# Optimization experiments

Measured on AMD Instinct MI355X. Metric: run time of the kernel, lower is better.

Reference implementation:

```python
import jax, jax.numpy as jnp
import numpy as np

B, CTX_DIM, CTX_SIZE, HID, SEQLEN = 32, 1024, 2048, 1024, 64


def setup_inputs() -> dict:
    key = jax.random.key(0)
    k1, k2, k3, k4 = jax.random.split(key, 4)
    hidden = jax.random.normal(k1, (1, B, HID), dtype=jnp.float32)
    contextvects = jax.random.normal(k2, (B, CTX_DIM, CTX_SIZE), dtype=jnp.float32)
    # nn.Linear(context_dim, hidden_size): W is [hidden_size, context_dim]
    W = jax.random.normal(k3, (HID, CTX_DIM), dtype=jnp.float32) / np.sqrt(CTX_DIM)
    b = jax.random.normal(k4, (HID,), dtype=jnp.float32) * 0.01
    return {"seqlen": SEQLEN, "hidden": hidden, "contextvects": contextvects, "W": W, "b": b}


def reference(seqlen, hidden, contextvects, W, b):
    # Original torch loop recomputes the identical quantities every timestep;
    # compute once and broadcast across seqlen (same math, no redundancy).
    # contextvects: [B, D, C]; project each context position: [B, C, H]
    context_proj = jnp.einsum('bdc,hd->bch', contextvects, W) + b
    # hidden: [1, B, H] -> scores [B, C]
    scores = jnp.einsum('bch,bh->bc', context_proj, hidden[0])
    attn_weights = jax.nn.softmax(scores, axis=1)  # softmax over context positions
    ctx = jnp.einsum('bdc,bc->bd', contextvects, attn_weights)  # [B, D]
    return jnp.broadcast_to(ctx[None, :, :], (seqlen, ctx.shape[0], ctx.shape[1]))
```

## Files before the change

### kernel.cpp

```cpp
#include <hip/hip_runtime.h>
#include <math.h>

#define NB 32
#define ND 1024
#define NC 2048
#define NH 1024
#define NSEQ 64
#define CCHUNK 32
#define NCHUNK (NC / CCHUNK)

__global__ __launch_bounds__(128) void k1_v(const float* __restrict__ hidden,
                                            const float* __restrict__ W,
                                            float* __restrict__ v) {
  const int b = blockIdx.x >> 3;
  const int d = ((blockIdx.x & 7) << 7) + threadIdx.x;
  const float* hb = hidden + b * NH;
  float acc = 0.f;
#pragma unroll 16
  for (int h = 0; h < NH; ++h) acc += hb[h] * W[h * ND + d];
  v[b * ND + d] = acc;
}

__global__ __launch_bounds__(256) void k2_main(const float* __restrict__ ctx,
                                               const float* __restrict__ v,
                                               float* __restrict__ accp,
                                               float* __restrict__ ml) {
  __shared__ __align__(16) float tile[ND * CCHUNK];
  __shared__ __align__(16) float vs[ND];
  __shared__ __align__(16) float4 sred[256];
  __shared__ __align__(16) float pf[CCHUNK];

  const int t = threadIdx.x;
  const int bid = blockIdx.x;
  const int b = bid >> 6;
  const int c0 = (bid & 63) * CCHUNK;

  {
    float4 vv = *(const float4*)(v + b * ND + t * 4);
    *(float4*)(vs + t * 4) = vv;
  }
  __syncthreads();

  const int cg = t & 7;
  const int dp = t >> 3;
  const float* gp = ctx + (size_t)b * ND * NC + (size_t)dp * NC + c0 + cg * 4;
  float* tw = tile + dp * CCHUNK + cg * 4;
  float4 s4 = make_float4(0.f, 0.f, 0.f, 0.f);
#pragma unroll 8
  for (int j = 0; j < 32; ++j) {
    float4 x = *(const float4*)(gp + (size_t)32 * NC * j);
    *(float4*)(tw + 32 * CCHUNK * j) = x;
    float vd = vs[dp + 32 * j];
    s4.x += x.x * vd; s4.y += x.y * vd; s4.z += x.z * vd; s4.w += x.w * vd;
  }
  sred[t] = s4;
  __syncthreads();

  if (t < 32) {
    const float* sr = (const float*)sred;
    float s = 0.f;
#pragma unroll
    for (int p = 0; p < 32; ++p) s += sr[p * 32 + t];
    float mm = s;
#pragma unroll
    for (int off = 16; off; off >>= 1) mm = fmaxf(mm, __shfl_xor(mm, off, 32));
    float e = __expf(s - mm);
    float ls = e;
#pragma unroll
    for (int off = 16; off; off >>= 1) ls += __shfl_xor(ls, off, 32);
    pf[t] = e;
    if (t == 0) { ml[bid * 2] = mm; ml[bid * 2 + 1] = ls; }
  }
  __syncthreads();

  float4 pr[8];
#pragma unroll
  for (int j = 0; j < 8; ++j)
    pr[j] = *(const float4*)(pf + ((j + t) & 7) * 4);

  float* ao = accp + (size_t)bid * ND;
#pragma unroll
  for (int k = 0; k < 4; ++k) {
    const int d = t + 256 * k;
    const float* tr = tile + d * CCHUNK;
    float a = 0.f;
#pragma unroll
    for (int j = 0; j < 8; ++j) {
      const int jr = (j + t) & 7;
      float4 x = *(const float4*)(tr + jr * 4);
      float4 pp = pr[j];
      a += x.x * pp.x + x.y * pp.y + x.z * pp.z + x.w * pp.w;
    }
    ao[d] = a;
  }
}

__global__ __launch_bounds__(256) void k3_combine(const float* __restrict__ accp,
                                                  const float* __restrict__ ml,
                                                  float* __restrict__ ctxo) {
  __shared__ float sc[64];
  __shared__ float sinv;
  const int b = blockIdx.x >> 2;
  const int dq = blockIdx.x & 3;
  const int t = threadIdx.x;
  if (t < 64) {
    float mi = ml[(b * 64 + t) * 2];
    float li = ml[(b * 64 + t) * 2 + 1];
    float mg = mi;
#pragma unroll
    for (int off = 32; off; off >>= 1) mg = fmaxf(mg, __shfl_xor(mg, off, 64));
    float scale = __expf(mi - mg);
    float dpart = scale * li;
#pragma unroll
    for (int off = 32; off; off >>= 1) dpart += __shfl_xor(dpart, off, 64);
    sc[t] = scale;
    if (t == 0) sinv = 1.0f / dpart;
  }
  __syncthreads();
  const int d = dq * 256 + t;
  const float* ap = accp + (size_t)b * 64 * ND + d;
  float acc = 0.f;
#pragma unroll 8
  for (int i = 0; i < 64; ++i) acc += sc[i] * ap[i * ND];
  ctxo[b * ND + d] = acc * sinv;
}

__global__ __launch_bounds__(256) void k4_bcast(const float* __restrict__ ctxo,
                                               float* __restrict__ out) {
  const int sb = blockIdx.x;
  const int b = sb & 31;
  const int t = threadIdx.x;
  float4 x = *(const float4*)(ctxo + b * ND + t * 4);
  *(float4*)(out + (size_t)sb * ND + t * 4) = x;
}

extern "C" void kernel_launch(void* const* d_in, const int* in_sizes, int n_in,
                              void* d_out, int out_size, void* d_ws, size_t ws_size,
                              hipStream_t stream) {
  (void)in_sizes; (void)n_in; (void)out_size; (void)ws_size;
  const float* hidden = (const float*)d_in[1];
  const float* ctxv   = (const float*)d_in[2];
  const float* W      = (const float*)d_in[3];
  float* out = (float*)d_out;

  char* ws = (char*)d_ws;
  float* v    = (float*)(ws);
  float* ml   = (float*)(ws + 131072);
  float* ctxo = (float*)(ws + 147456);

  k1_v<<<256, 128, 0, stream>>>(hidden, W, v);
  k2_main<<<NB * NCHUNK, 256, 0, stream>>>(ctxv, v, out, ml);
  k3_combine<<<128, 256, 0, stream>>>(out, ml, ctxo);
  k4_bcast<<<NSEQ * NB, 256, 0, stream>>>(ctxo, out);
}
```

Measured before the change: 424.3 us.

## Load context tiles directly to LDS, halve chunk size, fuse combine with broadcast

The main kernel now uses global_load_lds to stream context tiles straight into shared memory, with a chunk size of 16 positions instead of 32, which doubles the block count and halves LDS use per block. Hidden projections are held in registers rather than in shared memory. The combine and broadcast kernels are merged into one that writes all seqlen copies directly, and partial accumulators move to workspace instead of the output buffer, saving one launch and a round trip through memory. The tradeoff is twice as many partial vectors to combine, and a less parallel broadcast write spread over only 256 blocks.

Result: no change. 432.7 us (+2.0%).

```diff
diff --git a/kernel.cpp b/kernel.cpp
--- a/kernel.cpp
+++ b/kernel.cpp
@@ -6,8 +6,13 @@
 #define NC 2048
 #define NH 1024
 #define NSEQ 64
-#define CCHUNK 32
+#define CCHUNK 16
 #define NCHUNK (NC / CCHUNK)
+
+#define GLD_TO_LDS(g, l)                                                     \
+  __builtin_amdgcn_global_load_lds(                                          \
+      (const __attribute__((address_space(1))) void*)(g),                    \
+      (__attribute__((address_space(3))) void*)(l), 16, 0, 0)
 
 __global__ __launch_bounds__(128) void k1_v(const float* __restrict__ hidden,
                                             const float* __restrict__ W,
@@ -26,57 +31,60 @@
                                                float* __restrict__ accp,
                                                float* __restrict__ ml) {
   __shared__ __align__(16) float tile[ND * CCHUNK];
-  __shared__ __align__(16) float vs[ND];
-  __shared__ __align__(16) float4 sred[256];
+  __shared__ __align__(16) float sred[256 * 4];
   __shared__ __align__(16) float pf[CCHUNK];
 
   const int t = threadIdx.x;
   const int bid = blockIdx.x;
-  const int b = bid >> 6;
-  const int c0 = (bid & 63) * CCHUNK;
+  const int b = bid >> 7;
+  const int c0 = (bid & (NCHUNK - 1)) << 4;
+  const int dp = t >> 2;
+  const int cg = t & 3;
+  const int w = __builtin_amdgcn_readfirstlane(t >> 6);
 
-  {
-    float4 vv = *(const float4*)(v + b * ND + t * 4);
-    *(float4*)(vs + t * 4) = vv;
+  const float* gbase = ctx + (size_t)b * ND * NC + (size_t)dp * NC + c0 + cg * 4;
+#pragma unroll
+  for (int j = 0; j < 16; ++j) {
+    GLD_TO_LDS(gbase + (size_t)(64 * NC) * j, tile + j * 1024 + (w << 8));
+  }
+
+  float vsr[16];
+#pragma unroll
+  for (int j = 0; j < 16; ++j) vsr[j] = v[b * ND + dp + 64 * j];
+
+  __syncthreads();
+
+  float4 s4 = make_float4(0.f, 0.f, 0.f, 0.f);
+  const float* myw = tile + 4 * t;
+#pragma unroll
+  for (int j = 0; j < 16; ++j) {
+    float4 x = *(const float4*)(myw + j * 1024);
+    float vd = vsr[j];
+    s4.x += x.x * vd; s4.y += x.y * vd; s4.z += x.z * vd; s4.w += x.w * vd;
+  }
+  *(float4*)(sred + 4 * t) = s4;
+  __syncthreads();
+
+  if (t < 16) {
+    float s = 0.f;
+#pragma unroll
+    for (int q = 0; q < 64; ++q) s += sred[16 * q + t];
+    float mm = s;
+#pragma unroll
+    for (int off = 8; off; off >>= 1) mm = fmaxf(mm, __shfl_xor(mm, off, 16));
+    float e = __expf(s - mm);
+    float l = e;
+#pragma unroll
+    for (int off = 8; off; off >>= 1) l += __shfl_xor(l, off, 16);
+    pf[t] = e;
+    if (t == 0) { ml[bid * 2] = mm; ml[bid * 2 + 1] = l; }
   }
   __syncthreads();
 
-  const int cg = t & 7;
-  const int dp = t >> 3;
-  const float* gp = ctx + (size_t)b * ND * NC + (size_t)dp * NC + c0 + cg * 4;
-  float* tw = tile + dp * CCHUNK + cg * 4;
-  float4 s4 = make_float4(0.f, 0.f, 0.f, 0.f);
-#pragma unroll 8
-  for (int j = 0; j < 32; ++j) {
-    float4 x = *(const float4*)(gp + (size_t)32 * NC * j);
-    *(float4*)(tw + 32 * CCHUNK * j) = x;
-    float vd = vs[dp + 32 * j];
-    s4.x += x.x * vd; s4.y += x.y * vd; s4.z += x.z * vd; s4.w += x.w * vd;
-  }
-  sred[t] = s4;
-  __syncthreads();
-
-  if (t < 32) {
-    const float* sr = (const float*)sred;
-    float s = 0.f;
+  float4 pr[4];
 #pragma unroll
-    for (int p = 0; p < 32; ++p) s += sr[p * 32 + t];
-    float mm = s;
-#pragma unroll
-    for (int off = 16; off; off >>= 1) mm = fmaxf(mm, __shfl_xor(mm, off, 32));
-    float e = __expf(s - mm);
-    float ls = e;
-#pragma unroll
-    for (int off = 16; off; off >>= 1) ls += __shfl_xor(ls, off, 32);
-    pf[t] = e;
-    if (t == 0) { ml[bid * 2] = mm; ml[bid * 2 + 1] = ls; }
-  }
-  __syncthreads();
-
-  float4 pr[8];
-#pragma unroll
-  for (int j = 0; j < 8; ++j)
-    pr[j] = *(const float4*)(pf + ((j + t) & 7) * 4);
+  for (int j = 0; j < 4; ++j)
+    pr[j] = *(const float4*)(pf + (((j + t) & 3) << 2));
 
   float* ao = accp + (size_t)bid * ND;
 #pragma unroll
@@ -85,8 +93,8 @@
     const float* tr = tile + d * CCHUNK;
     float a = 0.f;
 #pragma unroll
-    for (int j = 0; j < 8; ++j) {
-      const int jr = (j + t) & 7;
+    for (int j = 0; j < 4; ++j) {
+      const int jr = (j + t) & 3;
       float4 x = *(const float4*)(tr + jr * 4);
       float4 pp = pr[j];
       a += x.x * pp.x + x.y * pp.y + x.z * pp.z + x.w * pp.w;
@@ -95,43 +103,43 @@
   }
 }
 
-__global__ __launch_bounds__(256) void k3_combine(const float* __restrict__ accp,
-                                                  const float* __restrict__ ml,
-                                                  float* __restrict__ ctxo) {
-  __shared__ float sc[64];
-  __shared__ float sinv;
-  const int b = blockIdx.x >> 2;
-  const int dq = blockIdx.x & 3;
+__global__ __launch_bounds__(128) void k3_combine_bcast(
+    const float* __restrict__ accp, const float* __restrict__ ml,
+    float* __restrict__ out) {
+  __shared__ float sc[NCHUNK];
+  __shared__ float red[4];
+  const int b = blockIdx.x >> 3;
+  const int dslice = blockIdx.x & 7;
   const int t = threadIdx.x;
-  if (t < 64) {
-    float mi = ml[(b * 64 + t) * 2];
-    float li = ml[(b * 64 + t) * 2 + 1];
-    float mg = mi;
+  const int w = t >> 6;
+
+  float mi = ml[(b * NCHUNK + t) * 2];
+  float li = ml[(b * NCHUNK + t) * 2 + 1];
+  float mg = mi;
 #pragma unroll
-    for (int off = 32; off; off >>= 1) mg = fmaxf(mg, __shfl_xor(mg, off, 64));
-    float scale = __expf(mi - mg);
-    float dpart = scale * li;
+  for (int off = 32; off; off >>= 1) mg = fmaxf(mg, __shfl_xor(mg, off, 64));
+  if ((t & 63) == 0) red[w] = mg;
+  __syncthreads();
+  mg = fmaxf(red[0], red[1]);
+  float scale = __expf(mi - mg);
+  float dpart = scale * li;
 #pragma unroll
-    for (int off = 32; off; off >>= 1) dpart += __shfl_xor(dpart, off, 64);
-    sc[t] = scale;
-    if (t == 0) sinv = 1.0f / dpart;
-  }
+  for (int off = 32; off; off >>= 1) dpart += __shfl_xor(dpart, off, 64);
+  sc[t] = scale;
+  if ((t & 63) == 0) red[2 + w] = dpart;
   __syncthreads();
-  const int d = dq * 256 + t;
-  const float* ap = accp + (size_t)b * 64 * ND + d;
+  const float sinv = 1.0f / (red[2] + red[3]);
+
+  const int d = dslice * 128 + t;
+  const float* ap = accp + (size_t)b * NCHUNK * ND + d;
   float acc = 0.f;
+#pragma unroll 16
+  for (int i = 0; i < NCHUNK; ++i) acc += sc[i] * ap[(size_t)i * ND];
+  acc *= sinv;
+
+  float* op = out + b * ND + d;
 #pragma unroll 8
-  for (int i = 0; i < 64; ++i) acc += sc[i] * ap[i * ND];
-  ctxo[b * ND + d] = acc * sinv;
-}
-
-__global__ __launch_bounds__(256) void k4_bcast(const float* __restrict__ ctxo,
-                                               float* __restrict__ out) {
-  const int sb = blockIdx.x;
-  const int b = sb & 31;
-  const int t = threadIdx.x;
-  float4 x = *(const float4*)(ctxo + b * ND + t * 4);
-  *(float4*)(out + (size_t)sb * ND + t * 4) = x;
+  for (int s = 0; s < NSEQ; ++s) op[(size_t)s * NB * ND] = acc;
 }
 
 extern "C" void kernel_launch(void* const* d_in, const int* in_sizes, int n_in,
@@ -146,10 +154,9 @@
   char* ws = (char*)d_ws;
   float* v    = (float*)(ws);
   float* ml   = (float*)(ws + 131072);
-  float* ctxo = (float*)(ws + 147456);
+  float* accp = (float*)(ws + 131072 + 32768);
 
   k1_v<<<256, 128, 0, stream>>>(hidden, W, v);
-  k2_main<<<NB * NCHUNK, 256, 0, stream>>>(ctxv, v, out, ml);
-  k3_combine<<<128, 256, 0, stream>>>(out, ml, ctxo);
-  k4_bcast<<<NSEQ * NB, 256, 0, stream>>>(ctxo, out);
+  k2_main<<<NB * NCHUNK, 256, 0, stream>>>(ctxv, v, accp, ml);
+  k3_combine_bcast<<<256, 128, 0, stream>>>(accp, ml, out);
 }
```
